# Kernel tuning notes

Measured on AMD Instinct MI355X. Metric: run time of the kernel, lower is better.

## Reference

```python
import jax, jax.numpy as jnp
import numpy as np
import math

VOCAB, EMBED, RES = 50257, 512, 2048
B, T = 64, 512
LN_EPS = 1e-5


def setup_inputs() -> dict:
    key = jax.random.key(0)
    k_x, k_e, k_r, k_w = jax.random.split(key, 4)
    x = jax.random.randint(k_x, (B, T), 0, VOCAB)
    embed_weight = jax.random.normal(k_e, (VOCAB, EMBED), dtype=jnp.float32)
    R = jax.random.normal(k_r, (RES, RES), dtype=jnp.float32) / math.sqrt(RES) / 0.9
    Win = jax.random.normal(k_w, (EMBED, RES), dtype=jnp.float32) / math.sqrt(EMBED) / 0.9
    gamma = jnp.ones((RES,), dtype=jnp.float32)
    beta = jnp.zeros((RES,), dtype=jnp.float32)
    return {"x": x, "embed_weight": embed_weight, "R": R, "Win": Win,
            "gamma": gamma, "beta": beta}


def reference(x, embed_weight, R, Win, gamma, beta):
    emb = embed_weight[x]                              # [B, T, E]
    inp = jnp.einsum('bte,er->btr', emb, Win)          # [B, T, RES]

    def step(state, u_t):                              # state: [B, RES]
        new_state = jnp.tanh(state @ R + u_t)
        return new_state, None

    state0 = jnp.zeros((x.shape[0], R.shape[0]), dtype=emb.dtype)
    state, _ = jax.lax.scan(step, state0, jnp.swapaxes(inp, 0, 1))  # scan over T

    # LayerNorm over last dim (eps=1e-5, affine)
    mu = jnp.mean(state, axis=-1, keepdims=True)
    var = jnp.mean((state - mu) ** 2, axis=-1, keepdims=True)
    normed = (state - mu) / jnp.sqrt(var + LN_EPS)
    return normed * gamma + beta
```

## Files before the change

kernel.cpp:

```cpp
#include <hip/hip_runtime.h>

#define BB 64
#define TT 512
#define EE 512
#define RR 2048
#define CPW 32
#define RPG 16
#define NWGS 256
#define FPAD 16
#define SLOT2 (BB * RR * 2)
#define GRP2  (RPG * RR * 2)
#define SPIN_CAP (1 << 20)

typedef _Float16 f16;
typedef f16 f16x8 __attribute__((ext_vector_type(8)));
typedef float f32x4 __attribute__((ext_vector_type(4)));

__device__ __forceinline__ float fast_tanh(float v) {
  float e = __expf(2.0f * v);
  return 1.0f - 2.0f / (e + 1.0f);
}

__device__ __forceinline__ void storeS(f16* p, f16 h) {
  union { f16 h; unsigned short s; } u;
  u.h = h;
  __hip_atomic_store((unsigned short*)p, u.s, __ATOMIC_RELAXED, __HIP_MEMORY_SCOPE_AGENT);
}

__device__ __forceinline__ unsigned flag_ld(const unsigned* p) {
  return __hip_atomic_load(p, __ATOMIC_RELAXED, __HIP_MEMORY_SCOPE_AGENT);
}
__device__ __forceinline__ void flag_st(unsigned* p, unsigned v) {
  __hip_atomic_store(p, v, __ATOMIC_RELAXED, __HIP_MEMORY_SCOPE_AGENT);
}

__device__ __forceinline__ void issue8(f16x8* dst, unsigned voff, const f16* sbase) {
#pragma unroll
  for (int i = 0; i < 8; ++i)
    asm volatile("global_load_dwordx4 %0, %1, %2 offset:%c3"
                 : "=v"(dst[i]) : "v"(voff), "s"(sbase), "i"(64 * i) : "memory");
}
__device__ __forceinline__ void issue16(f16x8* dst, unsigned voff, const f16* sbase) {
#pragma unroll
  for (int i = 0; i < 16; ++i)
    asm volatile("global_load_dwordx4 %0, %1, %2 offset:%c3"
                 : "=v"(dst[i]) : "v"(voff), "s"(sbase), "i"(64 * i) : "memory");
}

template <int N>
__device__ __forceinline__ void wait_vm() {
  asm volatile("s_waitcnt vmcnt(%c0)" :: "i"(N) : "memory");
  __builtin_amdgcn_sched_barrier(0);
}


__global__ void prep_emb(const int* __restrict__ x, const float* __restrict__ ew,
                         f16* __restrict__ emb) {
  const int row = blockIdx.x;
  const int tok = x[row];
  const float4* src = (const float4*)(ew + (size_t)tok * EE);
  f16* dst = emb + (size_t)row * EE;
  const int i = threadIdx.x;
  float4 v = src[i];
  union { f16 h[4]; unsigned long long u; } p;
  p.h[0] = (f16)v.x; p.h[1] = (f16)v.y; p.h[2] = (f16)v.z; p.h[3] = (f16)v.w;
  ((unsigned long long*)dst)[i] = p.u;
}

__global__ void prep_winT(const float* __restrict__ Win, f16* __restrict__ WinT) {
  const int i = blockIdx.x * blockDim.x + threadIdx.x;
  if (i < EE * RR) {
    const int k = i / RR, n = i % RR;
    WinT[(size_t)n * EE + k] = (f16)Win[i];
  }
}


__launch_bounds__(512, 1)
__global__ void scan_kernel(const float* __restrict__ R, f16* __restrict__ Sh,
                            const f16* __restrict__ emb, const f16* __restrict__ WinT,
                            unsigned* __restrict__ flg) {
  __shared__ __align__(16) char ldsbuf[CPW * RR * 2 + 16 * 1040 + 2 * RPG * CPW * 4];
  f16* Rt = (f16*)ldsbuf;
  const char* RtB = (const char*)ldsbuf;
  float* ubuf = (float*)(ldsbuf + CPW * RR * 2 + 16 * 1040);

  const int wg = blockIdx.x;
  const int xcd = wg & 7;
  const int grp = xcd >> 1;
  const int cw = ((wg >> 3) << 1) | (wg & 1);
  const int nbase = cw * CPW;
  const int rbase = grp * RPG;
  const int tid = threadIdx.x;
  const int wv = tid >> 6, l = tid & 63;
  unsigned* gflags = flg + (size_t)grp * 64 * FPAD;
  unsigned* myflag = gflags + cw * FPAD;
  f16* Sg = Sh + (size_t)grp * (RPG * RR);

  __builtin_amdgcn_fence(__ATOMIC_ACQUIRE, "agent");

  const int r16 = l & 15, kb = l >> 4;
  const int mm = tid >> 5, cc = tid & 31;

  {
    const int c = tid & 31, kst = tid >> 5;
    for (int k = kst; k < RR; k += 16) {
      const float v = R[(size_t)k * RR + nbase + c];
      const int idx = ((k >> 5) << 10) + ((c >> 4) << 9) +
                      (((c & 15) << 2) + ((k >> 3) & 3)) * 8 + (k & 7);
      Rt[idx] = (f16)v;
    }
  }

  f16x8 bfr[16];
  if (wv < 2) {
#pragma unroll
    for (int kc = 0; kc < 16; ++kc)
      bfr[kc] = *(const f16x8*)&WinT[(size_t)(nbase + wv * 16 + r16) * EE + kc * 32 + kb * 8];
  }
  __syncthreads();

  if (wv < 2) {
    f16x8 ebuf[16];
#pragma unroll
    for (int t01 = 0; t01 < 2; ++t01) {
      const unsigned ve = (unsigned)(((((rbase + r16) * TT) + t01) * EE + kb * 8) * 2);
      issue16(ebuf, ve, emb);
      wait_vm<0>();
      f32x4 au = {0.f, 0.f, 0.f, 0.f};
#pragma unroll
      for (int kc = 0; kc < 16; ++kc)
        au = __builtin_amdgcn_mfma_f32_16x16x32_f16(ebuf[kc], bfr[kc], au, 0, 0, 0);
#pragma unroll
      for (int j = 0; j < 4; ++j)
        ubuf[t01 * 512 + ((kb * 4 + j) * 32) + wv * 16 + r16] = au[j];
    }
  }
  __syncthreads();

  storeS(&Sg[(size_t)mm * RR + nbase + cc], (f16)fast_tanh(ubuf[mm * 32 + cc]));
  __syncthreads();
  if (tid == 0) flag_st(myflag, 1u);

  const int kblk = (wv + cw) & 7;
  const unsigned voffA = (unsigned)(((r16 * RR) + (kblk << 8) + kb * 8) * 2);
  const int bb0 = (r16 * 4 + kb) * 16;
  const int ntr = cc >> 4;
  const int lred = (cc & 15) | ((mm >> 2) << 4);
  const int jred = mm & 3;

  f16x8 abuf[8];

  for (int tau = 2; tau <= TT; ++tau) {
    const unsigned need = (unsigned)(tau - 1);

    {
      const unsigned* pp = &gflags[(size_t)(kblk * 8 + (l & 7)) * FPAD];
      unsigned fv = flag_ld(pp);
      int gd = 0;
      while (!__all(fv >= need) && ++gd < SPIN_CAP) {
        __builtin_amdgcn_s_sleep(1);
        fv = flag_ld(pp);
      }
    }

    const f16* sprev = Sh + (size_t)(tau - 2) * (BB * RR) + (size_t)grp * (RPG * RR);
    f16* snext = (f16*)((char*)Sh + (size_t)(tau - 1) * SLOT2) + (size_t)grp * (RPG * RR);

    issue8(abuf, voffA, sprev);

    f32x4 acc0 = {0.f, 0.f, 0.f, 0.f}, acc1 = {0.f, 0.f, 0.f, 0.f};
#define KSTEP(ks)                                                              \
  {                                                                            \
    const int kc = (kblk << 3) + (ks);                                         \
    f16x8 b0 = *(const f16x8*)(RtB + kc * 2048 + bb0);                         \
    f16x8 b1 = *(const f16x8*)(RtB + kc * 2048 + 1024 + bb0);                  \
    acc0 = __builtin_amdgcn_mfma_f32_16x16x32_f16(abuf[ks], b0, acc0, 0, 0, 0);\
    acc1 = __builtin_amdgcn_mfma_f32_16x16x32_f16(abuf[ks], b1, acc1, 0, 0, 0);\
  }
    wait_vm<4>();
    KSTEP(0) KSTEP(1) KSTEP(2) KSTEP(3)
    wait_vm<0>();
    KSTEP(4) KSTEP(5) KSTEP(6) KSTEP(7)
#undef KSTEP

    {
      char* red = ldsbuf + CPW * RR * 2;
      *(f32x4*)(red + (wv * 2 + 0) * 1040 + l * 16) = acc0;
      *(f32x4*)(red + (wv * 2 + 1) * 1040 + l * 16) = acc1;
    }
    __syncthreads();
    {
      const char* red = ldsbuf + CPW * RR * 2;
      float s = 0.f;
#pragma unroll
      for (int w = 0; w < 8; ++w)
        s += *(const float*)(red + (w * 2 + ntr) * 1040 + lred * 16 + jred * 4);
      const float uval = ubuf[((tau - 1) & 1) * 512 + mm * 32 + cc];
      storeS(&snext[(size_t)mm * RR + nbase + cc], (f16)fast_tanh(s + uval));
    }
    __syncthreads();
    if (tid == 0) flag_st(myflag, (unsigned)tau);

    if (wv < 2 && tau < TT) {
      f16x8 ebuf[16];
      const unsigned ve = (unsigned)(((((rbase + r16) * TT) + tau) * EE + kb * 8) * 2);
      issue16(ebuf, ve, emb);
      wait_vm<0>();
      f32x4 au = {0.f, 0.f, 0.f, 0.f};
#pragma unroll
      for (int kc = 0; kc < 16; ++kc)
        au = __builtin_amdgcn_mfma_f32_16x16x32_f16(ebuf[kc], bfr[kc], au, 0, 0, 0);
#pragma unroll
      for (int j = 0; j < 4; ++j)
        ubuf[(tau & 1) * 512 + ((kb * 4 + j) * 32) + wv * 16 + r16] = au[j];
    }
  }
}


__launch_bounds__(256, 1)
__global__ void ln_kernel(const char* __restrict__ slotbase, const float* __restrict__ gamma,
                          const float* __restrict__ beta, float* __restrict__ out) {
  const int b = blockIdx.x;
  const int tid = threadIdx.x;
  const f16* row = (const f16*)(slotbase + (size_t)(b >> 4) * GRP2) + (size_t)(b & 15) * RR;
  float vals[8];
  float lsum = 0.f, lsq = 0.f;
#pragma unroll
  for (int i = 0; i < 8; ++i) {
    float v = (float)row[tid + i * 256];
    vals[i] = v; lsum += v; lsq += v * v;
  }
#pragma unroll
  for (int off = 32; off >= 1; off >>= 1) {
    lsum += __shfl_xor(lsum, off);
    lsq  += __shfl_xor(lsq, off);
  }
  __shared__ float ps[4], pq[4];
  __shared__ float mu_s, rstd_s;
  const int wv = tid >> 6, l = tid & 63;
  if (l == 0) { ps[wv] = lsum; pq[wv] = lsq; }
  __syncthreads();
  if (tid == 0) {
    float s = 0.f, q = 0.f;
    for (int i = 0; i < 4; ++i) { s += ps[i]; q += pq[i]; }
    const float mu = s / RR;
    const float var = q / RR - mu * mu;
    mu_s = mu; rstd_s = rsqrtf(var + 1e-5f);
  }
  __syncthreads();
  const float mu = mu_s, rstd = rstd_s;
#pragma unroll
  for (int i = 0; i < 8; ++i) {
    const int idx = tid + i * 256;
    out[(size_t)b * RR + idx] = (vals[i] - mu) * rstd * gamma[idx] + beta[idx];
  }
}


extern "C" void kernel_launch(void* const* d_in, const int* in_sizes, int n_in,
                              void* d_out, int out_size, void* d_ws, size_t ws_size,
                              hipStream_t stream) {
  const int*   x     = (const int*)d_in[0];
  const float* ew    = (const float*)d_in[1];
  const float* Rm    = (const float*)d_in[2];
  const float* Win   = (const float*)d_in[3];
  const float* gamma = (const float*)d_in[4];
  const float* beta  = (const float*)d_in[5];

  const size_t SH_OFF  = 0;
  const size_t EMB_OFF = (size_t)TT * SLOT2;
  const size_t WT_OFF  = EMB_OFF + 33554432;
  const size_t FLG_OFF = WT_OFF + 2097152;
  const size_t NEED    = FLG_OFF + 16384;
  if (ws_size < NEED) {
    hipMemsetAsync(d_out, 0, (size_t)out_size * 4, stream);
    return;
  }
  char* ws = (char*)d_ws;
  f16*      Shist = (f16*)(ws + SH_OFF);
  f16*      emb   = (f16*)(ws + EMB_OFF);
  f16*      WinT  = (f16*)(ws + WT_OFF);
  unsigned* flg   = (unsigned*)(ws + FLG_OFF);

  hipMemsetAsync(flg, 0, 16384, stream);
  prep_emb<<<BB * TT, 128, 0, stream>>>(x, ew, emb);
  prep_winT<<<(EE * RR) / 256, 256, 0, stream>>>(Win, WinT);
  scan_kernel<<<NWGS, 512, 0, stream>>>(Rm, Shist, emb, WinT, flg);
  ln_kernel<<<BB, 256, 0, stream>>>(ws + (size_t)(TT - 1) * SLOT2,
                                    gamma, beta, (float*)d_out);
}
```

Baseline: 2.047 ms.

## Fuse input projection into recurrent MFMA accumulation across all waves

```diff
diff --git a/kernel.cpp b/kernel.cpp
--- a/kernel.cpp
+++ b/kernel.cpp
@@ -40,11 +40,11 @@
     asm volatile("global_load_dwordx4 %0, %1, %2 offset:%c3"
                  : "=v"(dst[i]) : "v"(voff), "s"(sbase), "i"(64 * i) : "memory");
 }
-__device__ __forceinline__ void issue16(f16x8* dst, unsigned voff, const f16* sbase) {
-#pragma unroll
-  for (int i = 0; i < 16; ++i)
-    asm volatile("global_load_dwordx4 %0, %1, %2 offset:%c3"
-                 : "=v"(dst[i]) : "v"(voff), "s"(sbase), "i"(64 * i) : "memory");
+__device__ __forceinline__ void issue2(f16x8* dst, unsigned voff, const f16* sbase) {
+  asm volatile("global_load_dwordx4 %0, %1, %2"
+               : "=v"(dst[0]) : "v"(voff), "s"(sbase) : "memory");
+  asm volatile("global_load_dwordx4 %0, %1, %2 offset:64"
+               : "=v"(dst[1]) : "v"(voff), "s"(sbase) : "memory");
 }
 
 template <int N>
@@ -80,10 +80,9 @@
 __global__ void scan_kernel(const float* __restrict__ R, f16* __restrict__ Sh,
                             const f16* __restrict__ emb, const f16* __restrict__ WinT,
                             unsigned* __restrict__ flg) {
-  __shared__ __align__(16) char ldsbuf[CPW * RR * 2 + 16 * 1040 + 2 * RPG * CPW * 4];
+  __shared__ __align__(16) char ldsbuf[CPW * RR * 2 + 16 * 1040];
   f16* Rt = (f16*)ldsbuf;
   const char* RtB = (const char*)ldsbuf;
-  float* ubuf = (float*)(ldsbuf + CPW * RR * 2 + 16 * 1040);
 
   const int wg = blockIdx.x;
   const int xcd = wg & 7;
@@ -101,6 +100,10 @@
 
   const int r16 = l & 15, kb = l >> 4;
   const int mm = tid >> 5, cc = tid & 31;
+  const int ntr = cc >> 4;
+  const int lred = (cc & 15) | ((mm >> 2) << 4);
+  const int jred = mm & 3;
+  char* red = ldsbuf + CPW * RR * 2;
 
   {
     const int c = tid & 31, kst = tid >> 5;
@@ -112,42 +115,42 @@
     }
   }
 
-  f16x8 bfr[16];
-  if (wv < 2) {
-#pragma unroll
-    for (int kc = 0; kc < 16; ++kc)
-      bfr[kc] = *(const f16x8*)&WinT[(size_t)(nbase + wv * 16 + r16) * EE + kc * 32 + kb * 8];
-  }
-  __syncthreads();
-
-  if (wv < 2) {
-    f16x8 ebuf[16];
-#pragma unroll
-    for (int t01 = 0; t01 < 2; ++t01) {
-      const unsigned ve = (unsigned)(((((rbase + r16) * TT) + t01) * EE + kb * 8) * 2);
-      issue16(ebuf, ve, emb);
-      wait_vm<0>();
-      f32x4 au = {0.f, 0.f, 0.f, 0.f};
-#pragma unroll
-      for (int kc = 0; kc < 16; ++kc)
-        au = __builtin_amdgcn_mfma_f32_16x16x32_f16(ebuf[kc], bfr[kc], au, 0, 0, 0);
-#pragma unroll
-      for (int j = 0; j < 4; ++j)
-        ubuf[t01 * 512 + ((kb * 4 + j) * 32) + wv * 16 + r16] = au[j];
-    }
-  }
-  __syncthreads();
-
-  storeS(&Sg[(size_t)mm * RR + nbase + cc], (f16)fast_tanh(ubuf[mm * 32 + cc]));
-  __syncthreads();
-  if (tid == 0) flag_st(myflag, 1u);
+  f16x8 wfr[2][2];
+#pragma unroll
+  for (int c2 = 0; c2 < 2; ++c2)
+#pragma unroll
+    for (int nt = 0; nt < 2; ++nt)
+      wfr[c2][nt] = *(const f16x8*)&WinT[(size_t)(nbase + nt * 16 + r16) * EE +
+                                         (2 * wv + c2) * 32 + kb * 8];
+
+  const unsigned voffE0 =
+      (unsigned)((((size_t)(rbase + r16) * TT) * EE + 2 * wv * 32 + kb * 8) * 2);
+
+  {
+    f16x8 ebuf[2];
+    issue2(ebuf, voffE0 , emb);
+    wait_vm<0>();
+    f32x4 a0 = {0.f, 0.f, 0.f, 0.f}, a1 = {0.f, 0.f, 0.f, 0.f};
+#pragma unroll
+    for (int c2 = 0; c2 < 2; ++c2) {
+      a0 = __builtin_amdgcn_mfma_f32_16x16x32_f16(ebuf[c2], wfr[c2][0], a0, 0, 0, 0);
+      a1 = __builtin_amdgcn_mfma_f32_16x16x32_f16(ebuf[c2], wfr[c2][1], a1, 0, 0, 0);
+    }
+    *(f32x4*)(red + (wv * 2 + 0) * 1040 + l * 16) = a0;
+    *(f32x4*)(red + (wv * 2 + 1) * 1040 + l * 16) = a1;
+    __syncthreads();
+    float s = 0.f;
+#pragma unroll
+    for (int w = 0; w < 8; ++w)
+      s += *(const float*)(red + (w * 2 + ntr) * 1040 + lred * 16 + jred * 4);
+    storeS(&Sg[(size_t)mm * RR + nbase + cc], (f16)fast_tanh(s));
+    __syncthreads();
+    if (tid == 0) flag_st(myflag, 1u);
+  }
 
   const int kblk = (wv + cw) & 7;
   const unsigned voffA = (unsigned)(((r16 * RR) + (kblk << 8) + kb * 8) * 2);
   const int bb0 = (r16 * 4 + kb) * 16;
-  const int ntr = cc >> 4;
-  const int lred = (cc & 15) | ((mm >> 2) << 4);
-  const int jred = mm & 3;
 
   f16x8 abuf[8];
 
@@ -168,6 +171,8 @@
     f16* snext = (f16*)((char*)Sh + (size_t)(tau - 1) * SLOT2) + (size_t)grp * (RPG * RR);
 
     issue8(abuf, voffA, sprev);
+    f16x8 ebuf[2];
+    issue2(ebuf, voffE0 + (unsigned)((tau - 1) * (EE * 2)), emb);
 
     f32x4 acc0 = {0.f, 0.f, 0.f, 0.f}, acc1 = {0.f, 0.f, 0.f, 0.f};
 #define KSTEP(ks)                                                              \
@@ -178,43 +183,30 @@
     acc0 = __builtin_amdgcn_mfma_f32_16x16x32_f16(abuf[ks], b0, acc0, 0, 0, 0);\
     acc1 = __builtin_amdgcn_mfma_f32_16x16x32_f16(abuf[ks], b1, acc1, 0, 0, 0);\
   }
-    wait_vm<4>();
+    wait_vm<6>();
     KSTEP(0) KSTEP(1) KSTEP(2) KSTEP(3)
-    wait_vm<0>();
+    wait_vm<2>();
     KSTEP(4) KSTEP(5) KSTEP(6) KSTEP(7)
 #undef KSTEP
-
+    wait_vm<0>();
+#pragma unroll
+    for (int c2 = 0; c2 < 2; ++c2) {
+      acc0 = __builtin_amdgcn_mfma_f32_16x16x32_f16(ebuf[c2], wfr[c2][0], acc0, 0, 0, 0);
+      acc1 = __builtin_amdgcn_mfma_f32_16x16x32_f16(ebuf[c2], wfr[c2][1], acc1, 0, 0, 0);
+    }
+
+    *(f32x4*)(red + (wv * 2 + 0) * 1040 + l * 16) = acc0;
+    *(f32x4*)(red + (wv * 2 + 1) * 1040 + l * 16) = acc1;
+    __syncthreads();
     {
-      char* red = ldsbuf + CPW * RR * 2;
-      *(f32x4*)(red + (wv * 2 + 0) * 1040 + l * 16) = acc0;
-      *(f32x4*)(red + (wv * 2 + 1) * 1040 + l * 16) = acc1;
-    }
-    __syncthreads();
-    {
-      const char* red = ldsbuf + CPW * RR * 2;
       float s = 0.f;
 #pragma unroll
       for (int w = 0; w < 8; ++w)
         s += *(const float*)(red + (w * 2 + ntr) * 1040 + lred * 16 + jred * 4);
-      const float uval = ubuf[((tau - 1) & 1) * 512 + mm * 32 + cc];
-      storeS(&snext[(size_t)mm * RR + nbase + cc], (f16)fast_tanh(s + uval));
+      storeS(&snext[(size_t)mm * RR + nbase + cc], (f16)fast_tanh(s));
     }
     __syncthreads();
     if (tid == 0) flag_st(myflag, (unsigned)tau);
-
-    if (wv < 2 && tau < TT) {
-      f16x8 ebuf[16];
-      const unsigned ve = (unsigned)(((((rbase + r16) * TT) + tau) * EE + kb * 8) * 2);
-      issue16(ebuf, ve, emb);
-      wait_vm<0>();
-      f32x4 au = {0.f, 0.f, 0.f, 0.f};
-#pragma unroll
-      for (int kc = 0; kc < 16; ++kc)
-        au = __builtin_amdgcn_mfma_f32_16x16x32_f16(ebuf[kc], bfr[kc], au, 0, 0, 0);
-#pragma unroll
-      for (int j = 0; j < 4; ++j)
-        ubuf[(tau & 1) * 512 + ((kb * 4 + j) * 32) + wv * 16 + r16] = au[j];
-    }
   }
 }
 
```

Result: faster. 1.962 ms (median of 2 runs) (-4.2%).
